# Performance work log

Hardware: AMD Instinct MI355X
Metric: run time of the kernel (lower is better)

## Reference

```python
import jax, jax.numpy as jnp
import numpy as np

WIN = (8, 7, 7)
SHIFT = (4, 3, 3)
HEADS = 4
DIM = 128
VOL = WIN[0] * WIN[1] * WIN[2]  # 392


def _rel_index():
    coords = np.stack(np.meshgrid(np.arange(WIN[0]), np.arange(WIN[1]), np.arange(WIN[2]), indexing='ij'))
    cf = coords.reshape(3, -1)
    rel = (cf[:, :, None] - cf[:, None, :]).transpose(1, 2, 0).astype(np.int64)
    rel[..., 0] += WIN[0] - 1
    rel[..., 1] += WIN[1] - 1
    rel[..., 2] += WIN[2] - 1
    rel[..., 0] *= (2 * WIN[1] - 1) * (2 * WIN[2] - 1)
    rel[..., 1] *= 2 * WIN[2] - 1
    return rel.sum(-1)  # [VOL, VOL]


def _attn_mask(tp, hp, wp):
    m = np.zeros((tp, hp, wp))
    slices = [((0, -WIN[i]), (-WIN[i], -SHIFT[i]), (-SHIFT[i], None)) for i in range(3)]
    cnt = 0
    for d in slices[0]:
        for h in slices[1]:
            for w in slices[2]:
                m[d[0]:d[1], h[0]:h[1], w[0]:w[1]] = cnt
                cnt += 1
    m = m.reshape(tp // WIN[0], WIN[0], hp // WIN[1], WIN[1], wp // WIN[2], WIN[2])
    m = m.transpose(0, 2, 4, 1, 3, 5).reshape(-1, VOL)  # [nW, VOL]
    diff = m[:, None, :] - m[:, :, None]
    return np.where(diff != 0, -100.0, 0.0).astype(np.float32)  # [nW, VOL, VOL]


_REL_IDX = _rel_index()


def setup_inputs() -> dict:
    key = jax.random.key(0)
    ks = jax.random.split(key, 6)
    return {
        'x': jax.random.normal(ks[0], (2, 16, 56, 56, DIM), dtype=jnp.float32),
        'qkv_weight': jax.random.normal(ks[1], (3 * DIM, DIM), dtype=jnp.float32) * 0.02,
        'qkv_bias': jax.random.normal(ks[2], (3 * DIM,), dtype=jnp.float32) * 0.02,
        'proj_weight': jax.random.normal(ks[3], (DIM, DIM), dtype=jnp.float32) * 0.02,
        'proj_bias': jax.random.normal(ks[4], (DIM,), dtype=jnp.float32) * 0.02,
        'rel_bias_table': jax.random.normal(ks[5], ((2 * WIN[0] - 1) * (2 * WIN[1] - 1) * (2 * WIN[2] - 1), HEADS), dtype=jnp.float32) * 0.02,
    }


def reference(x, qkv_weight, qkv_bias, proj_weight, proj_bias, rel_bias_table):
    b, t, h, w, c = x.shape
    hd = c // HEADS
    nt, nh, nw = t // WIN[0], h // WIN[1], w // WIN[2]
    NW = nt * nh * nw

    # relative position bias: [1, HEADS, VOL, VOL]
    bias = rel_bias_table[jnp.asarray(_REL_IDX.flatten())]
    bias = bias.reshape(VOL, VOL, HEADS).transpose(2, 0, 1)[None]

    # cyclic shift
    xs = jnp.roll(x, shift=(-SHIFT[0], -SHIFT[1], -SHIFT[2]), axis=(1, 2, 3))

    # window partition -> [B*NW, VOL, C]
    xw = xs.reshape(b, nt, WIN[0], nh, WIN[1], nw, WIN[2], c)
    xw = xw.transpose(0, 1, 3, 5, 2, 4, 6, 7).reshape(b * NW, VOL, c)

    qkv = xw @ qkv_weight.T + qkv_bias
    qkv = qkv.reshape(b * NW, VOL, 3, HEADS, hd).transpose(2, 0, 3, 1, 4)
    q, k, v = qkv[0] * (hd ** -0.5), qkv[1], qkv[2]

    attn = jnp.einsum('nhqd,nhkd->nhqk', q, k) + bias
    mask = jnp.asarray(_attn_mask(t, h, w))  # [NW, VOL, VOL]
    attn = attn.reshape(b, NW, HEADS, VOL, VOL) + mask[None, :, None]
    attn = jax.nn.softmax(attn, axis=-1).reshape(b * NW, HEADS, VOL, VOL)

    out = jnp.einsum('nhqk,nhkd->nqhd', attn, v).reshape(b * NW, VOL, c)
    out = out @ proj_weight.T + proj_bias

    # window reverse
    out = out.reshape(b, nt, nh, nw, WIN[0], WIN[1], WIN[2], c)
    out = out.transpose(0, 1, 4, 2, 5, 3, 6, 7).reshape(b, t, h, w, c)
    out = jnp.roll(out, shift=SHIFT, axis=(1, 2, 3))
    return out
```

## Files before the change

### kernel.cpp

```cpp
#include <hip/hip_runtime.h>


#define DIMC   128
#define HEADS  4
#define HD     32
#define VOL    392
#define VPAD   416
#define TQ     400
#define TK     416
#define SCALE2 0.25503490443f
#define LOG2E  1.4426950408889634f
#define MASK2  144.26950408889634f

typedef __bf16 bf16;
typedef __attribute__((ext_vector_type(8))) __bf16 bf16x8;
typedef __attribute__((ext_vector_type(4))) __bf16 bf16x4;
typedef __attribute__((ext_vector_type(2))) __bf16 bf16x2;
typedef __attribute__((ext_vector_type(4))) float  f32x4;

#define OFF_VT  (392*32)
#define VTCOLS  416
#define LDS_ELEMS (392*32 + 32*VTCOLS)
#define AW_BYTES  (256ull * VPAD * DIMC * 2ull)
#define TBL_BYTES (8ull * HEADS * TQ * TK * 2ull)

static __device__ inline bf16x8 pack8(float4 a, float4 b) {
    bf16x8 r;
    r[0] = (bf16)a.x; r[1] = (bf16)a.y; r[2] = (bf16)a.z; r[3] = (bf16)a.w;
    r[4] = (bf16)b.x; r[5] = (bf16)b.y; r[6] = (bf16)b.z; r[7] = (bf16)b.w;
    return r;
}
static __device__ inline bf16x8 zero8() {
    bf16x8 z;
#pragma unroll
    for (int i = 0; i < 8; ++i) z[i] = (bf16)0.0f;
    return z;
}
static __device__ inline bf16x8 ones8() {
    bf16x8 z;
#pragma unroll
    for (int i = 0; i < 8; ++i) z[i] = (bf16)1.0f;
    return z;
}
static __device__ inline int swz4(int row) { return ((row >> 1) ^ (row >> 3)) & 3; }

static __device__ inline unsigned pkbf(float a, float b) {
    bf16x2 t; t[0] = (bf16)a; t[1] = (bf16)b;
    return __builtin_bit_cast(unsigned, t);
}

#if defined(__has_builtin)
#if __has_builtin(__builtin_amdgcn_exp2f)
#define HAS_EXP2 1
#endif
#endif
static __device__ inline float exp2_hw(float x) {
#ifdef HAS_EXP2
    return __builtin_amdgcn_exp2f(x);
#else
    float r; asm volatile("v_exp_f32 %0, %1\n\ts_nop 0" : "=v"(r) : "v"(x)); return r;
#endif
}

__global__ __launch_bounds__(256) void gen_table(const float* __restrict__ btab,
                                                 bf16* __restrict__ tbl) {
    const int idx = blockIdx.x * 256 + threadIdx.x;
    const int total = 8 * HEADS * TQ * (TK / 4);
    if (idx >= total) return;
    const int k4  = (idx % (TK / 4)) * 4;
    const int q   = (idx / (TK / 4)) % TQ;
    const int h   = (idx / ((TK / 4) * TQ)) & 3;
    const int pat = idx / ((TK / 4) * TQ * HEADS);
    const int tb = (pat >> 2) & 1, hb = (pat >> 1) & 1, wb = pat & 1;

    int qt = 0, qh = 0, qw = 0, lq = 0;
    if (q < VOL) {
        qt = q / 49; const int qr = q - qt * 49; qh = qr / 7; qw = qr - qh * 7;
        lq = (tb ? (qt < 4 ? 1 : 2) : 0) * 9 + (hb ? (qh < 4 ? 1 : 2) : 0) * 3 +
             (wb ? (qw < 4 ? 1 : 2) : 0);
    }
    bf16x4 out;
#pragma unroll
    for (int j = 0; j < 4; ++j) {
        const int k = k4 + j;
        float v;
        if (k >= VOL)      v = -30000.0f;
        else if (q >= VOL) v = 0.0f;
        else {
            const int kt = k / 49; const int kr = k - kt * 49;
            const int kh = kr / 7; const int kw = kr - kh * 7;
            const int rel = ((qt - kt + 7) * 13 + (qh - kh + 6)) * 13 + (qw - kw + 6);
            v = btab[rel * HEADS + h] * LOG2E;
            const int lk = (tb ? (kt < 4 ? 1 : 2) : 0) * 9 +
                           (hb ? (kh < 4 ? 1 : 2) : 0) * 3 +
                           (wb ? (kw < 4 ? 1 : 2) : 0);
            if (lq != lk) v -= MASK2;
        }
        out[j] = (bf16)v;
    }
    *(bf16x4*)&tbl[((size_t)(pat * HEADS + h) * TQ + q) * TK + k4] = out;
}

__global__ __launch_bounds__(256) void conv_wproj(const float* __restrict__ wproj,
                                                  bf16* __restrict__ wpb) {
    const int i = (blockIdx.x * 256 + threadIdx.x) * 4;
    if (i < DIMC * DIMC) {
        float4 u = *(const float4*)(wproj + i);
        bf16x4 o; o[0] = (bf16)u.x; o[1] = (bf16)u.y; o[2] = (bf16)u.z; o[3] = (bf16)u.w;
        *(bf16x4*)(wpb + i) = o;
    }
}

#define NJ 7

__global__ __attribute__((amdgpu_flat_work_group_size(256, 256),
                          amdgpu_waves_per_eu(2, 4)))
void swin_attn(
    const float* __restrict__ x, const float* __restrict__ wqkv,
    const float* __restrict__ bqkv, const bf16* __restrict__ tbl,
    bf16* __restrict__ aw)
{
    __shared__ __align__(16) bf16 lds[LDS_ELEMS];

    const int bid  = blockIdx.x;
    const int xcd  = bid & 7;
    const int tt   = bid >> 3;
    const int win  = xcd * 32 + (tt >> 2);
    const int head = tt & 3;
    const int b    = win >> 7;
    const int wrem = win & 127;
    const int it   = wrem >> 6;
    const int ih   = (wrem >> 3) & 7;
    const int iw   = wrem & 7;
    const int pat  = ((it == 1) ? 4 : 0) | ((ih == 7) ? 2 : 0) | ((iw == 7) ? 1 : 0);

    const int tid  = threadIdx.x;
    const int lane = tid & 63;
    const int wv   = tid >> 6;
    const int l16  = lane & 15;
    const int lg   = lane >> 4;

    const bf16* tblh = tbl + (size_t)(pat * HEADS + head) * (TQ * TK);

    bf16x8 wfr[6][4];
    float  bcol[4];
#pragma unroll
    for (int o = 0; o < 6; ++o) {
        const int g = o >> 1, h2 = o & 1;
        const int wrow = g * DIMC + head * HD + h2 * 16 + l16;
        const float* wp = wqkv + (size_t)wrow * DIMC + 8 * lg;
#pragma unroll
        for (int ks = 0; ks < 4; ++ks)
            wfr[o][ks] = pack8(*(const float4*)(wp + ks * 32),
                               *(const float4*)(wp + ks * 32 + 4));
        if (o < 4) bcol[o] = bqkv[wrow];
    }
    float bvr[2][4];
#pragma unroll
    for (int h2 = 0; h2 < 2; ++h2)
#pragma unroll
        for (int r = 0; r < 4; ++r)
            bvr[h2][r] = bqkv[2 * DIMC + head * HD + h2 * 16 + lg * 4 + r];

    bf16x8 qf[NJ];
#pragma unroll
    for (int j = 0; j < NJ; ++j) qf[j] = zero8();

#pragma unroll
    for (int j = 0; j < NJ; ++j) {
        const int mt = wv + 4 * j;
        if (mt < 26) {
            const int tv = mt * 16 + l16;
            bf16x8 af[4];
            if (tv < VOL) {
                const int lt = tv / 49, rr = tv - lt * 49;
                const int lh = rr / 7,  lw = rr - lh * 7;
                const int t0 = (it * 8 + lt + 4) & 15;
                int h0 = ih * 7 + lh + 3; if (h0 >= 56) h0 -= 56;
                int w0 = iw * 7 + lw + 3; if (w0 >= 56) w0 -= 56;
                const float* xp = x + (size_t)(((b * 16 + t0) * 56 + h0) * 56 + w0) * DIMC + 8 * lg;
#pragma unroll
                for (int ks = 0; ks < 4; ++ks)
                    af[ks] = pack8(*(const float4*)(xp + ks * 32),
                                   *(const float4*)(xp + ks * 32 + 4));
            } else {
#pragma unroll
                for (int ks = 0; ks < 4; ++ks) af[ks] = zero8();
            }
#pragma unroll
            for (int o = 0; o < 2; ++o) {
                f32x4 acc = {0.f, 0.f, 0.f, 0.f};
#pragma unroll
                for (int ks = 0; ks < 4; ++ks)
                    acc = __builtin_amdgcn_mfma_f32_16x16x32_bf16(af[ks], wfr[o][ks], acc, 0, 0, 0);
                const int cb = (o & 1) * 16 + l16;
#pragma unroll
                for (int r = 0; r < 4; ++r) {
                    const int row = mt * 16 + lg * 4 + r;
                    if (row < VOL)
                        lds[row * 32 + (cb ^ (swz4(row) << 3))] = (bf16)((acc[r] + bcol[o]) * SCALE2);
                }
            }
            if (mt < 25) {
                const int qr = (tv < VOL) ? tv : (VOL - 1);
                qf[j] = *(const bf16x8*)&lds[qr * 32 + ((lg * 8) ^ (swz4(qr) << 3))];
            }
#pragma unroll
            for (int o = 2; o < 4; ++o) {
                f32x4 acc = {0.f, 0.f, 0.f, 0.f};
#pragma unroll
                for (int ks = 0; ks < 4; ++ks)
                    acc = __builtin_amdgcn_mfma_f32_16x16x32_bf16(af[ks], wfr[o][ks], acc, 0, 0, 0);
                const int cb = (o & 1) * 16 + l16;
#pragma unroll
                for (int r = 0; r < 4; ++r) {
                    const int row = mt * 16 + lg * 4 + r;
                    if (row < VOL)
                        lds[row * 32 + (cb ^ (swz4(row) << 3))] = (bf16)(acc[r] + bcol[o]);
                }
            }
#pragma unroll
            for (int h2 = 0; h2 < 2; ++h2) {
                f32x4 acc = {0.f, 0.f, 0.f, 0.f};
#pragma unroll
                for (int ks = 0; ks < 4; ++ks)
                    acc = __builtin_amdgcn_mfma_f32_16x16x32_bf16(wfr[4 + h2][ks], af[ks], acc, 0, 0, 0);
#pragma unroll
                for (int r = 0; r < 4; ++r) {
                    const int n = h2 * 16 + lg * 4 + r;
                    lds[OFF_VT + n * VTCOLS + (tv ^ (swz4(n) << 3))] = (bf16)(acc[r] + bvr[h2][r]);
                }
            }
        }
    }
    __syncthreads();

    {
        const int c = l16 & 3, d = l16 >> 2;
        const int rowA  = c + 8 * d;
        const int swzA  = (c >> 1) ^ d;
        const int swzB  = (2 + (c >> 1)) ^ d;
        const int kbA   = rowA * 32       + ((lg * 8) ^ (swzA << 3));
        const int kbB   = (rowA + 4) * 32 + ((lg * 8) ^ (swzB << 3));
        const int vb0   = OFF_VT + l16 * VTCOLS        + ((lg * 8) ^ (swz4(l16) << 3));
        const int vb1   = OFF_VT + (16 + l16) * VTCOLS + ((lg * 8) ^ (swz4(16 + l16) << 3));
        const bf16x8 onesf = ones8();

        int    tbOff[NJ];
        f32x4  o0[NJ], o1[NJ], sumv[NJ];
#pragma unroll
        for (int j = 0; j < NJ; ++j) {
            const int qtok = (wv + 4 * j) * 16 + l16;
            const int qc   = (qtok < TQ) ? qtok : (TQ - 1);
            tbOff[j] = (qc * TK + 8 * lg) * 2;
            o0[j]   = f32x4{0.f, 0.f, 0.f, 0.f};
            o1[j]   = f32x4{0.f, 0.f, 0.f, 0.f};
            sumv[j] = f32x4{0.f, 0.f, 0.f, 0.f};
        }

        uint4 bufA[NJ], bufB[NJ];
        bf16x8 kA0, kB0, v00, v10, kA1, kB1, v01, v11;

#define CH_PREB(CH, DST)                                                      \
        {                                                                     \
            const int chp_ = (CH) < 12 ? (CH) : 12;                           \
            _Pragma("unroll")                                                 \
            for (int j = 0; j < NJ; ++j)                                      \
                DST[j] = *(const uint4*)((const char*)tblh + tbOff[j] + chp_ * 64); \
        }
#define CH_PREF(CH, KA, KB, V0, V1)                                           \
        {                                                                     \
            const int chf_ = (CH) < 12 ? (CH) : 12;                           \
            KA = *(const bf16x8*)&lds[kbA + chf_ * 1024];                     \
            KB = *(const bf16x8*)&lds[kbB + chf_ * 1024];                     \
            V0 = *(const bf16x8*)&lds[vb0 + chf_ * 32];                       \
            V1 = *(const bf16x8*)&lds[vb1 + chf_ * 32];                       \
        }
#define CH_BODY(CUR, KA, KB, V0, V1)                                          \
        {                                                                     \
            __builtin_amdgcn_s_setprio(1);                                    \
            _Pragma("unroll")                                                 \
            for (int j = 0; j < NJ; ++j) {                                    \
                if (wv + 4 * j < 25) {                                        \
                    const uint4 bu = CUR[j];                                  \
                    f32x4 cA, cB;                                             \
                    cA[0] = __builtin_bit_cast(float, bu.x << 16);            \
                    cA[1] = __builtin_bit_cast(float, bu.x & 0xffff0000u);    \
                    cA[2] = __builtin_bit_cast(float, bu.y << 16);            \
                    cA[3] = __builtin_bit_cast(float, bu.y & 0xffff0000u);    \
                    cB[0] = __builtin_bit_cast(float, bu.z << 16);            \
                    cB[1] = __builtin_bit_cast(float, bu.z & 0xffff0000u);    \
                    cB[2] = __builtin_bit_cast(float, bu.w << 16);            \
                    cB[3] = __builtin_bit_cast(float, bu.w & 0xffff0000u);    \
                    const f32x4 sA = __builtin_amdgcn_mfma_f32_16x16x32_bf16(KA, qf[j], cA, 0, 0, 0); \
                    const f32x4 sB = __builtin_amdgcn_mfma_f32_16x16x32_bf16(KB, qf[j], cB, 0, 0, 0); \
                    union { unsigned u[4]; bf16x8 v; } pw;                    \
                    pw.u[0] = pkbf(exp2_hw(sA[0]), exp2_hw(sA[1]));           \
                    pw.u[1] = pkbf(exp2_hw(sA[2]), exp2_hw(sA[3]));           \
                    pw.u[2] = pkbf(exp2_hw(sB[0]), exp2_hw(sB[1]));           \
                    pw.u[3] = pkbf(exp2_hw(sB[2]), exp2_hw(sB[3]));           \
                    o0[j]   = __builtin_amdgcn_mfma_f32_16x16x32_bf16(V0, pw.v, o0[j], 0, 0, 0);   \
                    o1[j]   = __builtin_amdgcn_mfma_f32_16x16x32_bf16(V1, pw.v, o1[j], 0, 0, 0);   \
                    sumv[j] = __builtin_amdgcn_mfma_f32_16x16x32_bf16(onesf, pw.v, sumv[j], 0, 0, 0); \
                }                                                             \
            }                                                                 \
            __builtin_amdgcn_s_setprio(0);                                    \
        }

        CH_PREB(0, bufA)
        CH_PREF(0, kA0, kB0, v00, v10)

#pragma unroll 1
        for (int chp = 0; chp < 12; chp += 2) {
            CH_PREF(chp + 1, kA1, kB1, v01, v11)
            CH_PREB(chp + 1, bufB)
            CH_BODY(bufA, kA0, kB0, v00, v10)
            CH_PREF(chp + 2, kA0, kB0, v00, v10)
            CH_PREB(chp + 2, bufA)
            CH_BODY(bufB, kA1, kB1, v01, v11)
        }
        CH_BODY(bufA, kA0, kB0, v00, v10)
#undef CH_BODY
#undef CH_PREB
#undef CH_PREF

#pragma unroll
        for (int j = 0; j < NJ; ++j) {
            const int mt   = wv + 4 * j;
            const int qtok = mt * 16 + l16;
            if (mt < 25) {
                const float inv = 1.0f / sumv[j][0];
                if (qtok < VOL) {
                    bf16x4 w0, w1;
#pragma unroll
                    for (int r = 0; r < 4; ++r) {
                        w0[r] = (bf16)(o0[j][r] * inv);
                        w1[r] = (bf16)(o1[j][r] * inv);
                    }
                    bf16* op = aw + ((size_t)win * VPAD + qtok) * DIMC + head * HD + lg * 4;
                    *(bf16x4*)op = w0;
                    *(bf16x4*)(op + 16) = w1;
                }
            }
        }
    }
}

__global__ __launch_bounds__(256, 2) void swin_proj(
    const bf16* __restrict__ aw, const bf16* __restrict__ wpb,
    const float* __restrict__ bproj, float* __restrict__ out)
{
    const int bid  = blockIdx.x;
    const int xcd  = bid & 7;
    const int rest = bid >> 3;
    const int win  = xcd * 32 + (rest & 31);
    const int half = rest >> 5;
    const int b    = win >> 7;
    const int wrem = win & 127;
    const int it   = wrem >> 6;
    const int ih   = (wrem >> 3) & 7;
    const int iw   = wrem & 7;

    const int tid  = threadIdx.x;
    const int lane = tid & 63;
    const int wid  = tid >> 6;
    const int l16  = lane & 15;
    const int lg   = lane >> 4;

    const int mt_end = half ? 25 : 13;
    for (int mt = 13 * half + wid; mt < mt_end; mt += 4) {
        bf16x8 af[4];
        const bf16* ap = aw + ((size_t)win * VPAD + mt * 16 + l16) * DIMC + 8 * lg;
#pragma unroll
        for (int ks = 0; ks < 4; ++ks) af[ks] = *(const bf16x8*)(ap + ks * 32);

        float* ob[4]; bool qok[4];
#pragma unroll
        for (int r = 0; r < 4; ++r) {
            int q = mt * 16 + lg * 4 + r;
            qok[r] = q < VOL; if (!qok[r]) q = 0;
            const int lt = q / 49, rr = q - lt * 49;
            const int lh = rr / 7, lw = rr - lh * 7;
            const int t0 = (it * 8 + lt + 4) & 15;
            int h0 = ih * 7 + lh + 3; if (h0 >= 56) h0 -= 56;
            int w0 = iw * 7 + lw + 3; if (w0 >= 56) w0 -= 56;
            ob[r] = out + (size_t)(((b * 16 + t0) * 56 + h0) * 56 + w0) * DIMC;
        }
#pragma unroll
        for (int nt = 0; nt < 8; ++nt) {
            f32x4 acc = {0.f, 0.f, 0.f, 0.f};
            const bf16* wp = wpb + (size_t)(nt * 16 + l16) * DIMC + 8 * lg;
#pragma unroll
            for (int ks = 0; ks < 4; ++ks)
                acc = __builtin_amdgcn_mfma_f32_16x16x32_bf16(af[ks], *(const bf16x8*)(wp + ks * 32), acc, 0, 0, 0);
            const float bv = bproj[nt * 16 + l16];
#pragma unroll
            for (int r = 0; r < 4; ++r)
                if (qok[r]) ob[r][nt * 16 + l16] = acc[r] + bv;
        }
    }
}

extern "C" void kernel_launch(void* const* d_in, const int* in_sizes, int n_in,
                              void* d_out, int out_size, void* d_ws, size_t ws_size,
                              hipStream_t stream) {
    const float* x     = (const float*)d_in[0];
    const float* wqkv  = (const float*)d_in[1];
    const float* bqkv  = (const float*)d_in[2];
    const float* wproj = (const float*)d_in[3];
    const float* bproj = (const float*)d_in[4];
    const float* btab  = (const float*)d_in[5];
    bf16*  aw  = (bf16*)d_ws;
    bf16*  tbl = (bf16*)((char*)d_ws + AW_BYTES);
    bf16*  wpb = (bf16*)((char*)d_ws + AW_BYTES + TBL_BYTES);
    float* out = (float*)d_out;

    const int tbl_threads = 8 * HEADS * TQ * (TK / 4);
    gen_table<<<dim3((tbl_threads + 255) / 256), dim3(256), 0, stream>>>(btab, tbl);
    conv_wproj<<<dim3((DIMC * DIMC / 4 + 255) / 256), dim3(256), 0, stream>>>(wproj, wpb);
    swin_attn<<<dim3(1024), dim3(256), 0, stream>>>(x, wqkv, bqkv, tbl, aw);
    swin_proj<<<dim3(512), dim3(256), 0, stream>>>(aw, wpb, bproj, out);
}
```

Before: 119.4 us.

## Double-buffer x loads in QKV phase, fuse weight conversion, cap waves

```diff
diff --git a/kernel.cpp b/kernel.cpp
--- a/kernel.cpp
+++ b/kernel.cpp
@@ -63,8 +63,16 @@
 }
 
 __global__ __launch_bounds__(256) void gen_table(const float* __restrict__ btab,
-                                                 bf16* __restrict__ tbl) {
+                                                 bf16* __restrict__ tbl,
+                                                 const float* __restrict__ wproj,
+                                                 bf16* __restrict__ wpb) {
     const int idx = blockIdx.x * 256 + threadIdx.x;
+    if (idx < DIMC * DIMC / 4) {
+        const int i = idx * 4;
+        float4 u = *(const float4*)(wproj + i);
+        bf16x4 o; o[0] = (bf16)u.x; o[1] = (bf16)u.y; o[2] = (bf16)u.z; o[3] = (bf16)u.w;
+        *(bf16x4*)(wpb + i) = o;
+    }
     const int total = 8 * HEADS * TQ * (TK / 4);
     if (idx >= total) return;
     const int k4  = (idx % (TK / 4)) * 4;
@@ -101,20 +109,10 @@
     *(bf16x4*)&tbl[((size_t)(pat * HEADS + h) * TQ + q) * TK + k4] = out;
 }
 
-__global__ __launch_bounds__(256) void conv_wproj(const float* __restrict__ wproj,
-                                                  bf16* __restrict__ wpb) {
-    const int i = (blockIdx.x * 256 + threadIdx.x) * 4;
-    if (i < DIMC * DIMC) {
-        float4 u = *(const float4*)(wproj + i);
-        bf16x4 o; o[0] = (bf16)u.x; o[1] = (bf16)u.y; o[2] = (bf16)u.z; o[3] = (bf16)u.w;
-        *(bf16x4*)(wpb + i) = o;
-    }
-}
-
 #define NJ 7
 
 __global__ __attribute__((amdgpu_flat_work_group_size(256, 256),
-                          amdgpu_waves_per_eu(2, 4)))
+                          amdgpu_waves_per_eu(2, 2)))
 void swin_attn(
     const float* __restrict__ x, const float* __restrict__ wqkv,
     const float* __restrict__ bqkv, const bf16* __restrict__ tbl,
@@ -166,73 +164,98 @@
 #pragma unroll
     for (int j = 0; j < NJ; ++j) qf[j] = zero8();
 
-#pragma unroll
-    for (int j = 0; j < NJ; ++j) {
-        const int mt = wv + 4 * j;
-        if (mt < 26) {
-            const int tv = mt * 16 + l16;
-            bf16x8 af[4];
-            if (tv < VOL) {
-                const int lt = tv / 49, rr = tv - lt * 49;
-                const int lh = rr / 7,  lw = rr - lh * 7;
-                const int t0 = (it * 8 + lt + 4) & 15;
-                int h0 = ih * 7 + lh + 3; if (h0 >= 56) h0 -= 56;
-                int w0 = iw * 7 + lw + 3; if (w0 >= 56) w0 -= 56;
-                const float* xp = x + (size_t)(((b * 16 + t0) * 56 + h0) * 56 + w0) * DIMC + 8 * lg;
-#pragma unroll
-                for (int ks = 0; ks < 4; ++ks)
-                    af[ks] = pack8(*(const float4*)(xp + ks * 32),
-                                   *(const float4*)(xp + ks * 32 + 4));
-            } else {
-#pragma unroll
-                for (int ks = 0; ks < 4; ++ks) af[ks] = zero8();
-            }
-#pragma unroll
-            for (int o = 0; o < 2; ++o) {
-                f32x4 acc = {0.f, 0.f, 0.f, 0.f};
-#pragma unroll
-                for (int ks = 0; ks < 4; ++ks)
-                    acc = __builtin_amdgcn_mfma_f32_16x16x32_bf16(af[ks], wfr[o][ks], acc, 0, 0, 0);
-                const int cb = (o & 1) * 16 + l16;
-#pragma unroll
-                for (int r = 0; r < 4; ++r) {
-                    const int row = mt * 16 + lg * 4 + r;
-                    if (row < VOL)
-                        lds[row * 32 + (cb ^ (swz4(row) << 3))] = (bf16)((acc[r] + bcol[o]) * SCALE2);
-                }
-            }
-            if (mt < 25) {
-                const int qr = (tv < VOL) ? tv : (VOL - 1);
-                qf[j] = *(const bf16x8*)&lds[qr * 32 + ((lg * 8) ^ (swz4(qr) << 3))];
-            }
-#pragma unroll
-            for (int o = 2; o < 4; ++o) {
-                f32x4 acc = {0.f, 0.f, 0.f, 0.f};
-#pragma unroll
-                for (int ks = 0; ks < 4; ++ks)
-                    acc = __builtin_amdgcn_mfma_f32_16x16x32_bf16(af[ks], wfr[o][ks], acc, 0, 0, 0);
-                const int cb = (o & 1) * 16 + l16;
-#pragma unroll
-                for (int r = 0; r < 4; ++r) {
-                    const int row = mt * 16 + lg * 4 + r;
-                    if (row < VOL)
-                        lds[row * 32 + (cb ^ (swz4(row) << 3))] = (bf16)(acc[r] + bcol[o]);
-                }
-            }
-#pragma unroll
-            for (int h2 = 0; h2 < 2; ++h2) {
-                f32x4 acc = {0.f, 0.f, 0.f, 0.f};
-#pragma unroll
-                for (int ks = 0; ks < 4; ++ks)
-                    acc = __builtin_amdgcn_mfma_f32_16x16x32_bf16(wfr[4 + h2][ks], af[ks], acc, 0, 0, 0);
-#pragma unroll
-                for (int r = 0; r < 4; ++r) {
-                    const int n = h2 * 16 + lg * 4 + r;
-                    lds[OFF_VT + n * VTCOLS + (tv ^ (swz4(n) << 3))] = (bf16)(acc[r] + bvr[h2][r]);
-                }
-            }
-        }
-    }
+    float4 xr0[8], xr1[8];
+    bool   ok0 = false, ok1 = false;
+
+#define P1_LOAD(MT, XR, OK)                                                   \
+    {                                                                         \
+        const int mt_ = (MT);                                                 \
+        const int tv_ = mt_ * 16 + l16;                                       \
+        OK = (mt_ < 26) && (tv_ < VOL);                                       \
+        if (OK) {                                                             \
+            const int lt_ = tv_ / 49, rr_ = tv_ - lt_ * 49;                   \
+            const int lh_ = rr_ / 7, lw_ = rr_ - lh_ * 7;                     \
+            const int t0_ = (it * 8 + lt_ + 4) & 15;                          \
+            int h0_ = ih * 7 + lh_ + 3; if (h0_ >= 56) h0_ -= 56;             \
+            int w0_ = iw * 7 + lw_ + 3; if (w0_ >= 56) w0_ -= 56;             \
+            const float* xp_ = x + (size_t)(((b * 16 + t0_) * 56 + h0_) * 56 + w0_) * DIMC + 8 * lg; \
+            _Pragma("unroll")                                                 \
+            for (int u = 0; u < 8; ++u)                                       \
+                XR[u] = *(const float4*)(xp_ + (u >> 1) * 32 + (u & 1) * 4);  \
+        }                                                                     \
+    }
+#define P1_BODY(J, XR, OK)                                                    \
+    {                                                                         \
+        const int mt = wv + 4 * (J);                                          \
+        if (mt < 26) {                                                        \
+            const int tv = mt * 16 + l16;                                     \
+            bf16x8 af[4];                                                     \
+            _Pragma("unroll")                                                 \
+            for (int ks = 0; ks < 4; ++ks)                                    \
+                af[ks] = OK ? pack8(XR[2 * ks], XR[2 * ks + 1]) : zero8();    \
+            _Pragma("unroll")                                                 \
+            for (int o = 0; o < 2; ++o) {                                     \
+                f32x4 acc = {0.f, 0.f, 0.f, 0.f};                             \
+                _Pragma("unroll")                                             \
+                for (int ks = 0; ks < 4; ++ks)                                \
+                    acc = __builtin_amdgcn_mfma_f32_16x16x32_bf16(af[ks], wfr[o][ks], acc, 0, 0, 0); \
+                const int cb = (o & 1) * 16 + l16;                            \
+                _Pragma("unroll")                                             \
+                for (int r = 0; r < 4; ++r) {                                 \
+                    const int row = mt * 16 + lg * 4 + r;                     \
+                    if (row < VOL)                                            \
+                        lds[row * 32 + (cb ^ (swz4(row) << 3))] = (bf16)((acc[r] + bcol[o]) * SCALE2); \
+                }                                                             \
+            }                                                                 \
+            if (mt < 25) {                                                    \
+                const int qr = (tv < VOL) ? tv : (VOL - 1);                   \
+                qf[(J)] = *(const bf16x8*)&lds[qr * 32 + ((lg * 8) ^ (swz4(qr) << 3))]; \
+            }                                                                 \
+            _Pragma("unroll")                                                 \
+            for (int o = 2; o < 4; ++o) {                                     \
+                f32x4 acc = {0.f, 0.f, 0.f, 0.f};                             \
+                _Pragma("unroll")                                             \
+                for (int ks = 0; ks < 4; ++ks)                                \
+                    acc = __builtin_amdgcn_mfma_f32_16x16x32_bf16(af[ks], wfr[o][ks], acc, 0, 0, 0); \
+                const int cb = (o & 1) * 16 + l16;                            \
+                _Pragma("unroll")                                             \
+                for (int r = 0; r < 4; ++r) {                                 \
+                    const int row = mt * 16 + lg * 4 + r;                     \
+                    if (row < VOL)                                            \
+                        lds[row * 32 + (cb ^ (swz4(row) << 3))] = (bf16)(acc[r] + bcol[o]); \
+                }                                                             \
+            }                                                                 \
+            _Pragma("unroll")                                                 \
+            for (int h2 = 0; h2 < 2; ++h2) {                                  \
+                f32x4 acc = {0.f, 0.f, 0.f, 0.f};                             \
+                _Pragma("unroll")                                             \
+                for (int ks = 0; ks < 4; ++ks)                                \
+                    acc = __builtin_amdgcn_mfma_f32_16x16x32_bf16(wfr[4 + h2][ks], af[ks], acc, 0, 0, 0); \
+                _Pragma("unroll")                                             \
+                for (int r = 0; r < 4; ++r) {                                 \
+                    const int n = h2 * 16 + lg * 4 + r;                       \
+                    lds[OFF_VT + n * VTCOLS + (tv ^ (swz4(n) << 3))] = (bf16)(acc[r] + bvr[h2][r]); \
+                }                                                             \
+            }                                                                 \
+        }                                                                     \
+    }
+
+    P1_LOAD(wv, xr0, ok0)
+    P1_LOAD(wv + 4, xr1, ok1)
+    P1_BODY(0, xr0, ok0)
+    P1_LOAD(wv + 8, xr0, ok0)
+    P1_BODY(1, xr1, ok1)
+    P1_LOAD(wv + 12, xr1, ok1)
+    P1_BODY(2, xr0, ok0)
+    P1_LOAD(wv + 16, xr0, ok0)
+    P1_BODY(3, xr1, ok1)
+    P1_LOAD(wv + 20, xr1, ok1)
+    P1_BODY(4, xr0, ok0)
+    P1_LOAD(wv + 24, xr0, ok0)
+    P1_BODY(5, xr1, ok1)
+    P1_BODY(6, xr0, ok0)
+#undef P1_LOAD
+#undef P1_BODY
     __syncthreads();
 
     {
@@ -416,8 +439,7 @@
     float* out = (float*)d_out;
 
     const int tbl_threads = 8 * HEADS * TQ * (TK / 4);
-    gen_table<<<dim3((tbl_threads + 255) / 256), dim3(256), 0, stream>>>(btab, tbl);
-    conv_wproj<<<dim3((DIMC * DIMC / 4 + 255) / 256), dim3(256), 0, stream>>>(wproj, wpb);
+    gen_table<<<dim3((tbl_threads + 255) / 256), dim3(256), 0, stream>>>(btab, tbl, wproj, wpb);
     swin_attn<<<dim3(1024), dim3(256), 0, stream>>>(x, wqkv, bqkv, tbl, aw);
     swin_proj<<<dim3(512), dim3(256), 0, stream>>>(aw, wpb, bproj, out);
 }
```

New measurement: 114.9 us, median of 2. 3.8% less time.
